# Optimization experiments

Hardware: AMD Instinct MI355X
Metric: run time of the kernel (lower is better)

Reference implementation:

```python
import jax, jax.numpy as jnp
import numpy as np

B = 1024      # batch
DIN = 103     # generator/encoder input dim
L1, L2 = 64, 32   # encoder layer widths (latent = 32)
E = 8         # NUM_EXPERTS
GH = 64       # gating hidden width
H = 256       # generator hidden width
DOUT = 51     # generator output dim
EPS = 1e-5    # BatchNorm eps


def setup_inputs() -> dict:
    key = jax.random.key(0)
    ks = jax.random.split(key, 24)
    s = 0.05
    f32 = jnp.float32
    return {
        "x": jax.random.normal(ks[0], (B, DIN), f32),
        # encoder Linear + BN params
        "w1": jax.random.normal(ks[1], (L1, DIN), f32) * s,
        "b1": jnp.zeros((L1,), f32),
        "gamma1": jnp.ones((L1,), f32),
        "beta1": jnp.zeros((L1,), f32),
        "w2": jax.random.normal(ks[2], (L2, L1), f32) * s,
        "b2": jnp.zeros((L2,), f32),
        "gamma2": jnp.ones((L2,), f32),
        "beta2": jnp.zeros((L2,), f32),
        # gating MLP (latent 32 -> GH -> GH -> E, ELU, softmax)
        "gw1": jax.random.normal(ks[3], (GH, L2), f32) * s,
        "gb1": jnp.zeros((GH,), f32),
        "gw2": jax.random.normal(ks[4], (GH, GH), f32) * s,
        "gb2": jnp.zeros((GH,), f32),
        "gw3": jax.random.normal(ks[5], (E, GH), f32) * s,
        "gb3": jnp.zeros((E,), f32),
        # expert weight banks for 3-layer generator (MANN style)
        "ew1": jax.random.normal(ks[6], (E, DIN, H), f32) * s,
        "eb1": jnp.zeros((E, H), f32),
        "ew2": jax.random.normal(ks[7], (E, H, H), f32) * s,
        "eb2": jnp.zeros((E, H), f32),
        "ew3": jax.random.normal(ks[8], (E, H, DOUT), f32) * s,
        "eb3": jnp.zeros((E, DOUT), f32),
    }


def _batchnorm(h, gamma, beta):
    # training-mode BatchNorm1d: per-batch mean/var (biased var, matching torch)
    m = jnp.mean(h, axis=0)
    v = jnp.mean((h - m) ** 2, axis=0)
    return gamma * (h - m) * jax.lax.rsqrt(v + EPS) + beta


def reference(x, w1, b1, gamma1, beta1, w2, b2, gamma2, beta2,
              gw1, gb1, gw2, gb2, gw3, gb3,
              ew1, eb1, ew2, eb2, ew3, eb3):
    # in-place scale of last 3 features (x[:,100:103] *= 100)
    xs = x.at[:, 100:103].multiply(100.0)
    # encoder: Linear -> BN -> ReLU, twice
    h = jax.nn.relu(_batchnorm(xs @ w1.T + b1, gamma1, beta1))
    latent = jax.nn.relu(_batchnorm(h @ w2.T + b2, gamma2, beta2))
    # gating network -> blending coefficients BC [B, E]
    g = jax.nn.elu(latent @ gw1.T + gb1)
    g = jax.nn.elu(g @ gw2.T + gb2)
    bc = jax.nn.softmax(g @ gw3.T + gb3, axis=-1)
    # MANN-style generator: per-sample expert-blended weights
    wb1 = jnp.einsum('be,eih->bih', bc, ew1)   # [B, DIN, H]
    h1 = jax.nn.elu(jnp.einsum('bi,bih->bh', xs, wb1) + bc @ eb1)
    wb2 = jnp.einsum('be,ehk->bhk', bc, ew2)   # [B, H, H]
    h2 = jax.nn.elu(jnp.einsum('bh,bhk->bk', h1, wb2) + bc @ eb2)
    wb3 = jnp.einsum('be,eho->bho', bc, ew3)   # [B, H, DOUT]
    out = jnp.einsum('bh,bho->bo', h2, wb3) + bc @ eb3
    return out
```

## Files before the change

### kernel.cpp

```cpp
#include <hip/hip_runtime.h>
#include <math.h>


#define DIN 103
#define NE  8
#define HH  256
#define DOUT 51
#define EPSBN 1e-5f

typedef __attribute__((ext_vector_type(8))) short bf16x8;
typedef __attribute__((ext_vector_type(4))) float f32x4;
typedef __attribute__((ext_vector_type(8))) unsigned short us8;
typedef unsigned short ushort_t;

__device__ __forceinline__ float eluf(float v) { return v > 0.f ? v : (expf(v) - 1.f); }
__device__ __forceinline__ unsigned short bf16h(float f) {
  unsigned u = __float_as_uint(f);
  u += 0x7FFFu + ((u >> 16) & 1u);
  return (unsigned short)(u >> 16);
}
__device__ __forceinline__ float bf16f(unsigned short h) { return __uint_as_float(((unsigned)h) << 16); }
__device__ __forceinline__ void split_bf16(float v, unsigned short& h, unsigned short& l) {
  h = bf16h(v);
  l = bf16h(v - bf16f(h));
}
#define MFMA __builtin_amdgcn_mfma_f32_16x16x32_bf16

#define O_SLOTS1 0
#define O_SLOTS2 8192
#define O_H1RAW  20480
#define O_H2RAW  86016
#define O_XSH    118784
#define O_XSL    184320
#define O_E1H    258048
#define O_E1L    389120
#define O_E2H    520192
#define O_E3H    782336

__global__ __launch_bounds__(256) void k_prep_enc1(
    const float* __restrict__ x, const float* __restrict__ w1, const float* __restrict__ b1,
    const float* __restrict__ ew1, const float* __restrict__ ew2, const float* __restrict__ ew3,
    float* __restrict__ ws) {
  __shared__ union {
    float tile[32][65];
    float xt[16][104];
    struct { float w1L[64 * DIN]; float xr[16][104]; float hb[16][64]; } e1;
  } sm;
  int bk = blockIdx.x, t = threadIdx.x;
  int l2 = t & 63, c = l2 & 15, q = l2 >> 4;

  if (bk < 256) {
    int nh = bk & 3, kc = (bk >> 2) & 7, e = bk >> 5;
    int k0 = kc * 32, n0 = nh * 64;
#pragma unroll
    for (int i = 0; i < 8; ++i) {
      int kl = (t >> 6) + i * 4;
      sm.tile[kl][t & 63] = ew2[((size_t)e * HH + k0 + kl) * HH + n0 + (t & 63)];
    }
    __syncthreads();
    int nsl = t >> 6;
    us8 H8;
#pragma unroll
    for (int j = 0; j < 8; ++j) H8[j] = bf16h(sm.tile[q * 8 + j][nsl * 16 + c]);
    size_t dst = (((size_t)(e * 16 + nh * 4 + nsl)) * 8 + kc) * 512 + l2 * 8;
    *(us8*)((ushort_t*)(ws + O_E2H) + dst) = H8;
  } else if (bk < 384) {
    int b2 = bk - 256;
    int nh = b2 & 3, kc = (b2 >> 2) & 3, e = b2 >> 4;
    int k0 = kc * 32, n0 = nh * 64;
#pragma unroll
    for (int i = 0; i < 8; ++i) {
      int kl = (t >> 6) + i * 4;
      int k = k0 + kl;
      sm.tile[kl][t & 63] = (k < DIN) ? ew1[((size_t)e * DIN + k) * HH + n0 + (t & 63)] : 0.f;
    }
    __syncthreads();
    int nsl = t >> 6;
    us8 H8, L8;
#pragma unroll
    for (int j = 0; j < 8; ++j) {
      unsigned short h, lo; split_bf16(sm.tile[q * 8 + j][nsl * 16 + c], h, lo);
      H8[j] = h; L8[j] = lo;
    }
    size_t dst = (((size_t)(e * 16 + nh * 4 + nsl)) * 4 + kc) * 512 + l2 * 8;
    *(us8*)((ushort_t*)(ws + O_E1H) + dst) = H8;
    *(us8*)((ushort_t*)(ws + O_E1L) + dst) = L8;
  } else if (bk < 448) {
    int b2 = bk - 384;
    int kc = b2 & 7, e = b2 >> 3;
    int k0 = kc * 32;
#pragma unroll
    for (int i = 0; i < 8; ++i) {
      int kl = (t >> 6) + i * 4;
      int n = t & 63;
      sm.tile[kl][n] = (n < DOUT) ? ew3[((size_t)e * HH + k0 + kl) * DOUT + n] : 0.f;
    }
    __syncthreads();
    int nsl = t >> 6;
    us8 H8;
#pragma unroll
    for (int j = 0; j < 8; ++j) H8[j] = bf16h(sm.tile[q * 8 + j][nsl * 16 + c]);
    size_t dst = (((size_t)(e * 4 + nsl)) * 8 + kc) * 512 + l2 * 8;
    *(us8*)((ushort_t*)(ws + O_E3H) + dst) = H8;
  } else if (bk < 512) {
    int msub = bk - 448;
    for (int i = t; i < 16 * 104; i += 256) {
      int b = i / 104, k = i - b * 104;
      float v = 0.f;
      if (k < DIN) { v = x[(size_t)(msub * 16 + b) * DIN + k]; if (k >= 100) v *= 100.f; }
      sm.xt[b][k] = v;
    }
    __syncthreads();
    int kc = t >> 6;
    int m = c;
    us8 H8, L8;
#pragma unroll
    for (int j = 0; j < 8; ++j) {
      int k = kc * 32 + q * 8 + j;
      float v = (k < 104) ? sm.xt[m][k] : 0.f;
      unsigned short h, lo; split_bf16(v, h, lo);
      H8[j] = h; L8[j] = lo;
    }
    size_t dst = ((size_t)msub * 4 + kc) * 512 + l2 * 8;
    *(us8*)((ushort_t*)(ws + O_XSH) + dst) = H8;
    *(us8*)((ushort_t*)(ws + O_XSL) + dst) = L8;
  } else {
    float* slots1 = ws + O_SLOTS1;
    float* h1raw  = ws + O_H1RAW;
    int bkl = bk - 512;
    int r0 = bkl * 16;
    for (int i = t; i < 64 * DIN; i += 256) sm.e1.w1L[i] = w1[i];
    for (int i = t; i < 16 * 104; i += 256) {
      int r = i / 104, c2 = i - r * 104;
      float v = 0.f;
      if (c2 < DIN) { v = x[(size_t)(r0 + r) * DIN + c2]; if (c2 >= 100) v *= 100.f; }
      sm.e1.xr[r][c2] = v;
    }
    __syncthreads();
#pragma unroll
    for (int i = 0; i < 4; ++i) {
      int idx = t + i * 256;
      int r = idx >> 6, j = idx & 63;
      float acc = b1[j];
      for (int k = 0; k < DIN; ++k) acc = fmaf(sm.e1.xr[r][k], sm.e1.w1L[j * DIN + k], acc);
      sm.e1.hb[r][j] = acc;
      h1raw[(size_t)(r0 + r) * 64 + j] = acc;
    }
    __syncthreads();
    if (t < 64) {
      float s = 0.f, qq = 0.f;
      for (int r = 0; r < 16; ++r) { float v = sm.e1.hb[r][t]; s += v; qq += v * v; }
      slots1[bkl * 128 + t] = s;
      slots1[bkl * 128 + 64 + t] = qq;
    }
  }
}

__global__ __launch_bounds__(256) void k_enc2(
    const float* __restrict__ gamma1, const float* __restrict__ beta1,
    const float* __restrict__ w2, const float* __restrict__ b2, float* __restrict__ ws) {
  __shared__ float w2T[64 * 33];
  __shared__ float red[128];
  __shared__ float sc1[64], sh1[64];
  __shared__ float h1b[16][64];
  __shared__ float hb2[16][32];
  float* slots1 = ws + O_SLOTS1;
  float* slots2 = ws + O_SLOTS2;
  float* h1raw  = ws + O_H1RAW;
  float* h2raw  = ws + O_H2RAW;
  int bk = blockIdx.x, t = threadIdx.x;
  int R0 = bk * 16;
  for (int i = t; i < 2048; i += 256) { int j = i >> 6, k = i & 63; w2T[k * 33 + j] = w2[i]; }
  if (t < 128) {
    float s = 0.f;
    for (int b = 0; b < 64; ++b) s += slots1[b * 128 + t];
    red[t] = s;
  }
  __syncthreads();
  if (t < 64) {
    float m = red[t] * (1.f / 1024.f);
    float v = red[64 + t] * (1.f / 1024.f) - m * m;
    float sc = gamma1[t] * rsqrtf(v + EPSBN);
    sc1[t] = sc; sh1[t] = beta1[t] - m * sc;
  }
  __syncthreads();
#pragma unroll
  for (int i = 0; i < 4; ++i) {
    int idx = t + i * 256;
    int r = idx >> 6, k = idx & 63;
    h1b[r][k] = fmaxf(fmaf(h1raw[(size_t)(R0 + r) * 64 + k], sc1[k], sh1[k]), 0.f);
  }
  __syncthreads();
#pragma unroll
  for (int i = 0; i < 2; ++i) {
    int o = t + i * 256;
    int r = o >> 5, j = o & 31;
    float acc = b2[j];
    for (int k = 0; k < 64; ++k) acc = fmaf(h1b[r][k], w2T[k * 33 + j], acc);
    hb2[r][j] = acc;
    h2raw[(size_t)(R0 + r) * 32 + j] = acc;
  }
  __syncthreads();
  if (t < 32) {
    float s = 0.f, q = 0.f;
    for (int r = 0; r < 16; ++r) { float v = hb2[r][t]; s += v; q += v * v; }
    slots2[bk * 64 + t] = s;
    slots2[bk * 64 + 32 + t] = q;
  }
}

__global__ __launch_bounds__(512) void k_mega(
    const float* __restrict__ gamma2, const float* __restrict__ beta2,
    const float* __restrict__ gw1, const float* __restrict__ gb1,
    const float* __restrict__ gw2, const float* __restrict__ gb2,
    const float* __restrict__ gw3, const float* __restrict__ gb3,
    const float* __restrict__ eb1, const float* __restrict__ eb2,
    const float* __restrict__ eb3,
    const float* __restrict__ ws, float* __restrict__ out) {
  __shared__ union {
    struct {
      float gw1L[64 * 33];
      float gw2L[64 * 65];
      float gw3L[8 * 65];
      float gb1L[64], gb2L[64], gb3L[8];
      float red2[64], sc2[32], sh2[32];
      float lat[16][32];
      float g1[16][64], g2[16][64];
    } gate;
    struct {
      float hT[256][17];
      float eb[2048];
    } comb;
    struct {
      float p3s[8][16][64];
      float eb3L[8][64];
    } g3;
  } U;
  __shared__ us8 aHv[512], aLv[512];
  __shared__ float bcL[16][8];

  const int bk = blockIdx.x, t = threadIdx.x;
  const int wv = t >> 6, l = t & 63, c = l & 15, quad = l >> 4;
  const int R0 = bk * 16;
  const float* slots2 = ws + O_SLOTS2;
  const float* h2raw  = ws + O_H2RAW;
  const ushort_t* XsH = (const ushort_t*)(ws + O_XSH);
  const ushort_t* XsL = (const ushort_t*)(ws + O_XSL);
  const ushort_t* E1H = (const ushort_t*)(ws + O_E1H);
  const ushort_t* E1L = (const ushort_t*)(ws + O_E1L);
  const ushort_t* E2H = (const ushort_t*)(ws + O_E2H);
  const ushort_t* E3H = (const ushort_t*)(ws + O_E3H);

  for (int i = t; i < 2048; i += 512) { int j = i >> 5, k = i & 31; U.gate.gw1L[j * 33 + k] = gw1[i]; }
  for (int i = t; i < 4096; i += 512) { int j = i >> 6, k = i & 63; U.gate.gw2L[j * 65 + k] = gw2[i]; }
  { int j = t >> 6, k = t & 63; U.gate.gw3L[j * 65 + k] = gw3[t]; }
  if (t < 64) { U.gate.gb1L[t] = gb1[t]; U.gate.gb2L[t] = gb2[t]; }
  if (t < 8) U.gate.gb3L[t] = gb3[t];
  if (t < 64) {
    float s = 0.f;
    for (int b = 0; b < 64; ++b) s += slots2[b * 64 + t];
    U.gate.red2[t] = s;
  }
  __syncthreads();
  if (t < 32) {
    float m = U.gate.red2[t] * (1.f / 1024.f);
    float v = U.gate.red2[32 + t] * (1.f / 1024.f) - m * m;
    float sc = gamma2[t] * rsqrtf(v + EPSBN);
    U.gate.sc2[t] = sc; U.gate.sh2[t] = beta2[t] - m * sc;
  }
  __syncthreads();
  { int r = t >> 5, cc = t & 31;
    U.gate.lat[r][cc] = fmaxf(fmaf(h2raw[(size_t)(R0 + r) * 32 + cc], U.gate.sc2[cc], U.gate.sh2[cc]), 0.f); }
  __syncthreads();
#pragma unroll
  for (int rr = 0; rr < 2; ++rr) {
    int r = wv * 2 + rr;
    float a1 = U.gate.gb1L[l];
    for (int k = 0; k < 32; ++k) a1 = fmaf(U.gate.gw1L[l * 33 + k], U.gate.lat[r][k], a1);
    U.gate.g1[r][l] = eluf(a1);
  }
  __syncthreads();
#pragma unroll
  for (int rr = 0; rr < 2; ++rr) {
    int r = wv * 2 + rr;
    float a2 = U.gate.gb2L[l];
    for (int k = 0; k < 64; ++k) a2 = fmaf(U.gate.gw2L[l * 65 + k], U.gate.g1[r][k], a2);
    U.gate.g2[r][l] = eluf(a2);
  }
  __syncthreads();
#pragma unroll
  for (int rr = 0; rr < 2; ++rr) {
    int r = wv * 2 + rr;
    if (l < 8) {
      float a3 = U.gate.gb3L[l];
      for (int k = 0; k < 64; ++k) a3 = fmaf(U.gate.gw3L[l * 65 + k], U.gate.g2[r][k], a3);
      float mx = a3;
      mx = fmaxf(mx, __shfl_xor(mx, 1));
      mx = fmaxf(mx, __shfl_xor(mx, 2));
      mx = fmaxf(mx, __shfl_xor(mx, 4));
      float p = expf(a3 - mx);
      float sp = p;
      sp += __shfl_xor(sp, 1); sp += __shfl_xor(sp, 2); sp += __shfl_xor(sp, 4);
      bcL[r][l] = p / sp;
    }
  }
  __syncthreads();

  for (int i = t; i < 2048; i += 512) U.comb.eb[i] = eb1[i];
  bf16x8 a1h[4], a1l[4];
#pragma unroll
  for (int kc = 0; kc < 4; ++kc) {
    a1h[kc] = *(const bf16x8*)(XsH + ((size_t)bk * 4 + kc) * 512 + l * 8);
    a1l[kc] = *(const bf16x8*)(XsL + ((size_t)bk * 4 + kc) * 512 + l * 8);
  }
  __syncthreads();
  {
    f32x4 blend[2] = {};
#pragma unroll
    for (int e = 0; e < NE; ++e) {
      float bcv[4];
#pragma unroll
      for (int r = 0; r < 4; ++r) bcv[r] = bcL[quad * 4 + r][e];
#pragma unroll
      for (int nsi = 0; nsi < 2; ++nsi) {
        int ns = wv * 2 + nsi;
        f32x4 acc = {};
#pragma unroll
        for (int kc = 0; kc < 4; ++kc) {
          size_t bo = (((size_t)(e * 16 + ns)) * 4 + kc) * 512 + l * 8;
          bf16x8 bh = *(const bf16x8*)(E1H + bo);
          bf16x8 bl = *(const bf16x8*)(E1L + bo);
          acc = MFMA(a1h[kc], bh, acc, 0, 0, 0);
          acc = MFMA(a1l[kc], bh, acc, 0, 0, 0);
          acc = MFMA(a1h[kc], bl, acc, 0, 0, 0);
        }
        float ebv = U.comb.eb[e * HH + ns * 16 + c];
#pragma unroll
        for (int r = 0; r < 4; ++r) blend[nsi][r] = fmaf(bcv[r], acc[r] + ebv, blend[nsi][r]);
      }
    }
#pragma unroll
    for (int nsi = 0; nsi < 2; ++nsi) {
      int col = (wv * 2 + nsi) * 16 + c;
#pragma unroll
      for (int r = 0; r < 4; ++r) U.comb.hT[col][quad * 4 + r] = eluf(blend[nsi][r]);
    }
  }
  __syncthreads();
  {
    int l2 = t & 63, row = l2 & 15, k0 = (t >> 6) * 32 + (l2 >> 4) * 8;
    us8 H, L;
#pragma unroll
    for (int j = 0; j < 8; ++j) {
      unsigned short h, lo; split_bf16(U.comb.hT[k0 + j][row], h, lo);
      H[j] = h; L[j] = lo;
    }
    aHv[t] = H; aLv[t] = L;
  }
  __syncthreads();

  for (int i = t; i < 2048; i += 512) U.comb.eb[i] = eb2[i];
  bf16x8 a2h[8], a2l[8];
#pragma unroll
  for (int kc = 0; kc < 8; ++kc) {
    a2h[kc] = *(const bf16x8*)&aHv[kc * 64 + l];
    a2l[kc] = *(const bf16x8*)&aLv[kc * 64 + l];
  }
  __syncthreads();
  {
    f32x4 blend[2] = {};
#pragma unroll
    for (int e = 0; e < NE; ++e) {
      float bcv[4];
#pragma unroll
      for (int r = 0; r < 4; ++r) bcv[r] = bcL[quad * 4 + r][e];
#pragma unroll
      for (int nsi = 0; nsi < 2; ++nsi) {
        int ns = wv * 2 + nsi;
        f32x4 acc = {};
#pragma unroll
        for (int kc = 0; kc < 8; ++kc) {
          size_t bo = (((size_t)(e * 16 + ns)) * 8 + kc) * 512 + l * 8;
          bf16x8 bh = *(const bf16x8*)(E2H + bo);
          acc = MFMA(a2h[kc], bh, acc, 0, 0, 0);
          acc = MFMA(a2l[kc], bh, acc, 0, 0, 0);
        }
        float ebv = U.comb.eb[e * HH + ns * 16 + c];
#pragma unroll
        for (int r = 0; r < 4; ++r) blend[nsi][r] = fmaf(bcv[r], acc[r] + ebv, blend[nsi][r]);
      }
    }
#pragma unroll
    for (int nsi = 0; nsi < 2; ++nsi) {
      int col = (wv * 2 + nsi) * 16 + c;
#pragma unroll
      for (int r = 0; r < 4; ++r) U.comb.hT[col][quad * 4 + r] = eluf(blend[nsi][r]);
    }
  }
  __syncthreads();
  {
    int l2 = t & 63, row = l2 & 15, k0 = (t >> 6) * 32 + (l2 >> 4) * 8;
    us8 H, L;
#pragma unroll
    for (int j = 0; j < 8; ++j) {
      unsigned short h, lo; split_bf16(U.comb.hT[k0 + j][row], h, lo);
      H[j] = h; L[j] = lo;
    }
    aHv[t] = H; aLv[t] = L;
  }
  __syncthreads();

  { int e = t >> 6, n = t & 63; U.g3.eb3L[e][n] = (n < DOUT) ? eb3[e * DOUT + n] : 0.f; }
  {
    const int e = wv;
    f32x4 acc[4] = {};
#pragma unroll
    for (int kc = 0; kc < 8; ++kc) {
      bf16x8 ah = *(const bf16x8*)&aHv[kc * 64 + l];
      bf16x8 al = *(const bf16x8*)&aLv[kc * 64 + l];
#pragma unroll
      for (int nsi = 0; nsi < 4; ++nsi) {
        size_t bo = (((size_t)(e * 4 + nsi)) * 8 + kc) * 512 + l * 8;
        bf16x8 bh = *(const bf16x8*)(E3H + bo);
        acc[nsi] = MFMA(ah, bh, acc[nsi], 0, 0, 0);
        acc[nsi] = MFMA(al, bh, acc[nsi], 0, 0, 0);
      }
    }
#pragma unroll
    for (int nsi = 0; nsi < 4; ++nsi)
#pragma unroll
      for (int r = 0; r < 4; ++r)
        U.g3.p3s[e][quad * 4 + r][nsi * 16 + c] = acc[nsi][r];
  }
  __syncthreads();
#pragma unroll
  for (int i = 0; i < 2; ++i) {
    int idx = t + i * 512;
    int row = idx >> 6, col = idx & 63;
    float s = 0.f;
#pragma unroll
    for (int e2 = 0; e2 < 8; ++e2)
      s = fmaf(bcL[row][e2], U.g3.p3s[e2][row][col] + U.g3.eb3L[e2][col], s);
    if (col < DOUT) out[(size_t)(R0 + row) * DOUT + col] = s;
  }
}

extern "C" void kernel_launch(void* const* d_in, const int* in_sizes, int n_in,
                              void* d_out, int out_size, void* d_ws, size_t ws_size,
                              hipStream_t stream) {
  const float* x      = (const float*)d_in[0];
  const float* w1     = (const float*)d_in[1];
  const float* b1     = (const float*)d_in[2];
  const float* gamma1 = (const float*)d_in[3];
  const float* beta1  = (const float*)d_in[4];
  const float* w2     = (const float*)d_in[5];
  const float* b2     = (const float*)d_in[6];
  const float* gamma2 = (const float*)d_in[7];
  const float* beta2  = (const float*)d_in[8];
  const float* gw1    = (const float*)d_in[9];
  const float* gb1    = (const float*)d_in[10];
  const float* gw2    = (const float*)d_in[11];
  const float* gb2    = (const float*)d_in[12];
  const float* gw3    = (const float*)d_in[13];
  const float* gb3    = (const float*)d_in[14];
  const float* ew1    = (const float*)d_in[15];
  const float* eb1    = (const float*)d_in[16];
  const float* ew2    = (const float*)d_in[17];
  const float* eb2    = (const float*)d_in[18];
  const float* ew3    = (const float*)d_in[19];
  const float* eb3    = (const float*)d_in[20];
  float* wsf  = (float*)d_ws;
  float* outp = (float*)d_out;

  k_prep_enc1<<<576, 256, 0, stream>>>(x, w1, b1, ew1, ew2, ew3, wsf);
  k_enc2<<<64, 256, 0, stream>>>(gamma1, beta1, w2, b2, wsf);
  k_mega<<<64, 512, 0, stream>>>(gamma2, beta2, gw1, gb1, gw2, gb2, gw3, gb3,
                                 eb1, eb2, eb3, wsf, outp);
}
```

Before: 156.7 us.

## Fuse enc2 into mega kernel via software grid barrier and L2 prefetch

Removes the separate enc2 kernel launch by computing the second encoder layer inside the mega kernel. A hierarchical atomic grid barrier across the 64 blocks makes the BN2 batch statistics complete before gating starts, and the pre-BN h2 values now stay in shared memory instead of going through global memory. Before the barrier, each block reads a slice of the expert weight workspace into a discarded sum so those weights are warm in cache. The change relies on all 64 blocks being co-resident, which holds at this grid size, and adds barrier spin time plus extra reads for the prefetch.

```diff
diff --git a/kernel.cpp b/kernel.cpp
--- a/kernel.cpp
+++ b/kernel.cpp
@@ -26,16 +26,50 @@
 }
 #define MFMA __builtin_amdgcn_mfma_f32_16x16x32_bf16
 
+__device__ __forceinline__ void stA(float* p, float v) {
+  __hip_atomic_store(p, v, __ATOMIC_RELAXED, __HIP_MEMORY_SCOPE_AGENT);
+}
+__device__ __forceinline__ float ldA(const float* p) {
+  return __hip_atomic_load((float*)p, __ATOMIC_RELAXED, __HIP_MEMORY_SCOPE_AGENT);
+}
+__device__ __forceinline__ void stAu(unsigned* p, unsigned v) {
+  __hip_atomic_store(p, v, __ATOMIC_RELAXED, __HIP_MEMORY_SCOPE_AGENT);
+}
+__device__ __forceinline__ unsigned ldAu(const unsigned* p) {
+  return __hip_atomic_load((unsigned*)p, __ATOMIC_RELAXED, __HIP_MEMORY_SCOPE_AGENT);
+}
+
 #define O_SLOTS1 0
 #define O_SLOTS2 8192
 #define O_H1RAW  20480
-#define O_H2RAW  86016
 #define O_XSH    118784
 #define O_XSL    184320
 #define O_E1H    258048
 #define O_E1L    389120
 #define O_E2H    520192
 #define O_E3H    782336
+#define O_ESPAN  589824
+#define O_BAR    1372160
+
+__device__ __forceinline__ void gbar64(unsigned* base, int blk) {
+  asm volatile("s_waitcnt vmcnt(0)" ::: "memory");
+  __syncthreads();
+  if (threadIdx.x == 0) {
+    unsigned a = __hip_atomic_fetch_add(base + (blk >> 3) * 32, 1u,
+                                        __ATOMIC_RELAXED, __HIP_MEMORY_SCOPE_AGENT);
+    if (a == 7u) {
+      unsigned r = __hip_atomic_fetch_add(base + 256, 1u,
+                                          __ATOMIC_RELAXED, __HIP_MEMORY_SCOPE_AGENT);
+      if (r == 7u) {
+#pragma unroll
+        for (int j = 0; j < 8; ++j) stAu(base + 288 + j * 32, 1u);
+      }
+    }
+    while (ldAu(base + 288 + (blk & 7) * 32) == 0u)
+      __builtin_amdgcn_s_sleep(2);
+  }
+  __syncthreads();
+}
 
 __global__ __launch_bounds__(256) void k_prep_enc1(
     const float* __restrict__ x, const float* __restrict__ w1, const float* __restrict__ b1,
@@ -48,6 +82,11 @@
   } sm;
   int bk = blockIdx.x, t = threadIdx.x;
   int l2 = t & 63, c = l2 & 15, q = l2 >> 4;
+  if (bk == 0) {
+    unsigned* bz = (unsigned*)(ws + O_BAR);
+#pragma unroll
+    for (int i = 0; i < 4; ++i) bz[t + i * 256] = 0u;
+  }
 
   if (bk < 256) {
     int nh = bk & 3, kc = (bk >> 2) & 7, e = bk >> 5;
@@ -156,94 +195,34 @@
   }
 }
 
-__global__ __launch_bounds__(256) void k_enc2(
+__global__ __launch_bounds__(512) void k_mega(
     const float* __restrict__ gamma1, const float* __restrict__ beta1,
-    const float* __restrict__ w2, const float* __restrict__ b2, float* __restrict__ ws) {
-  __shared__ float w2T[64 * 33];
-  __shared__ float red[128];
-  __shared__ float sc1[64], sh1[64];
-  __shared__ float h1b[16][64];
-  __shared__ float hb2[16][32];
-  float* slots1 = ws + O_SLOTS1;
-  float* slots2 = ws + O_SLOTS2;
-  float* h1raw  = ws + O_H1RAW;
-  float* h2raw  = ws + O_H2RAW;
-  int bk = blockIdx.x, t = threadIdx.x;
-  int R0 = bk * 16;
-  for (int i = t; i < 2048; i += 256) { int j = i >> 6, k = i & 63; w2T[k * 33 + j] = w2[i]; }
-  if (t < 128) {
-    float s = 0.f;
-    for (int b = 0; b < 64; ++b) s += slots1[b * 128 + t];
-    red[t] = s;
-  }
-  __syncthreads();
-  if (t < 64) {
-    float m = red[t] * (1.f / 1024.f);
-    float v = red[64 + t] * (1.f / 1024.f) - m * m;
-    float sc = gamma1[t] * rsqrtf(v + EPSBN);
-    sc1[t] = sc; sh1[t] = beta1[t] - m * sc;
-  }
-  __syncthreads();
-#pragma unroll
-  for (int i = 0; i < 4; ++i) {
-    int idx = t + i * 256;
-    int r = idx >> 6, k = idx & 63;
-    h1b[r][k] = fmaxf(fmaf(h1raw[(size_t)(R0 + r) * 64 + k], sc1[k], sh1[k]), 0.f);
-  }
-  __syncthreads();
-#pragma unroll
-  for (int i = 0; i < 2; ++i) {
-    int o = t + i * 256;
-    int r = o >> 5, j = o & 31;
-    float acc = b2[j];
-    for (int k = 0; k < 64; ++k) acc = fmaf(h1b[r][k], w2T[k * 33 + j], acc);
-    hb2[r][j] = acc;
-    h2raw[(size_t)(R0 + r) * 32 + j] = acc;
-  }
-  __syncthreads();
-  if (t < 32) {
-    float s = 0.f, q = 0.f;
-    for (int r = 0; r < 16; ++r) { float v = hb2[r][t]; s += v; q += v * v; }
-    slots2[bk * 64 + t] = s;
-    slots2[bk * 64 + 32 + t] = q;
-  }
-}
-
-__global__ __launch_bounds__(512) void k_mega(
+    const float* __restrict__ w2, const float* __restrict__ b2,
     const float* __restrict__ gamma2, const float* __restrict__ beta2,
     const float* __restrict__ gw1, const float* __restrict__ gb1,
     const float* __restrict__ gw2, const float* __restrict__ gb2,
     const float* __restrict__ gw3, const float* __restrict__ gb3,
     const float* __restrict__ eb1, const float* __restrict__ eb2,
     const float* __restrict__ eb3,
-    const float* __restrict__ ws, float* __restrict__ out) {
+    float* __restrict__ ws, float* __restrict__ out) {
   __shared__ union {
-    struct {
-      float gw1L[64 * 33];
-      float gw2L[64 * 65];
-      float gw3L[8 * 65];
-      float gb1L[64], gb2L[64], gb3L[8];
-      float red2[64], sc2[32], sh2[32];
-      float lat[16][32];
-      float g1[16][64], g2[16][64];
-    } gate;
-    struct {
-      float hT[256][17];
-      float eb[2048];
-    } comb;
-    struct {
-      float p3s[8][16][64];
-      float eb3L[8][64];
-    } g3;
+    struct { float w2T[64 * 33]; float red[128]; float sc1[64], sh1[64];
+             float h1b[16][64]; } enc2;
+    struct { float gw1L[64 * 33]; float gw2L[64 * 65]; float gw3L[8 * 65];
+             float gb1L[64], gb2L[64], gb3L[8];
+             float red2[64], sc2[32], sh2[32];
+             float lat[16][32]; float g1[16][64], g2[16][64]; } gate;
+    struct { float hT[256][17]; float eb[2048]; } comb;
+    struct { float p3s[8][16][64]; float eb3L[8][64]; } g3;
   } U;
+  __shared__ float hb2s[16][32];
   __shared__ us8 aHv[512], aLv[512];
   __shared__ float bcL[16][8];
 
-  const int bk = blockIdx.x, t = threadIdx.x;
+  const int blk = blockIdx.x, t = threadIdx.x;
   const int wv = t >> 6, l = t & 63, c = l & 15, quad = l >> 4;
-  const int R0 = bk * 16;
-  const float* slots2 = ws + O_SLOTS2;
-  const float* h2raw  = ws + O_H2RAW;
+  const int R0 = blk * 16;
+  unsigned* bar = (unsigned*)(ws + O_BAR);
   const ushort_t* XsH = (const ushort_t*)(ws + O_XSH);
   const ushort_t* XsL = (const ushort_t*)(ws + O_XSL);
   const ushort_t* E1H = (const ushort_t*)(ws + O_E1H);
@@ -251,167 +230,230 @@
   const ushort_t* E2H = (const ushort_t*)(ws + O_E2H);
   const ushort_t* E3H = (const ushort_t*)(ws + O_E3H);
 
-  for (int i = t; i < 2048; i += 512) { int j = i >> 5, k = i & 31; U.gate.gw1L[j * 33 + k] = gw1[i]; }
-  for (int i = t; i < 4096; i += 512) { int j = i >> 6, k = i & 63; U.gate.gw2L[j * 65 + k] = gw2[i]; }
-  { int j = t >> 6, k = t & 63; U.gate.gw3L[j * 65 + k] = gw3[t]; }
-  if (t < 64) { U.gate.gb1L[t] = gb1[t]; U.gate.gb2L[t] = gb2[t]; }
-  if (t < 8) U.gate.gb3L[t] = gb3[t];
-  if (t < 64) {
-    float s = 0.f;
-    for (int b = 0; b < 64; ++b) s += slots2[b * 64 + t];
-    U.gate.red2[t] = s;
-  }
-  __syncthreads();
-  if (t < 32) {
-    float m = U.gate.red2[t] * (1.f / 1024.f);
-    float v = U.gate.red2[32 + t] * (1.f / 1024.f) - m * m;
-    float sc = gamma2[t] * rsqrtf(v + EPSBN);
-    U.gate.sc2[t] = sc; U.gate.sh2[t] = beta2[t] - m * sc;
-  }
-  __syncthreads();
-  { int r = t >> 5, cc = t & 31;
-    U.gate.lat[r][cc] = fmaxf(fmaf(h2raw[(size_t)(R0 + r) * 32 + cc], U.gate.sc2[cc], U.gate.sh2[cc]), 0.f); }
-  __syncthreads();
-#pragma unroll
-  for (int rr = 0; rr < 2; ++rr) {
-    int r = wv * 2 + rr;
-    float a1 = U.gate.gb1L[l];
-    for (int k = 0; k < 32; ++k) a1 = fmaf(U.gate.gw1L[l * 33 + k], U.gate.lat[r][k], a1);
-    U.gate.g1[r][l] = eluf(a1);
-  }
-  __syncthreads();
-#pragma unroll
-  for (int rr = 0; rr < 2; ++rr) {
-    int r = wv * 2 + rr;
-    float a2 = U.gate.gb2L[l];
-    for (int k = 0; k < 64; ++k) a2 = fmaf(U.gate.gw2L[l * 65 + k], U.gate.g1[r][k], a2);
-    U.gate.g2[r][l] = eluf(a2);
-  }
-  __syncthreads();
-#pragma unroll
-  for (int rr = 0; rr < 2; ++rr) {
-    int r = wv * 2 + rr;
-    if (l < 8) {
-      float a3 = U.gate.gb3L[l];
-      for (int k = 0; k < 64; ++k) a3 = fmaf(U.gate.gw3L[l * 65 + k], U.gate.g2[r][k], a3);
-      float mx = a3;
-      mx = fmaxf(mx, __shfl_xor(mx, 1));
-      mx = fmaxf(mx, __shfl_xor(mx, 2));
-      mx = fmaxf(mx, __shfl_xor(mx, 4));
-      float p = expf(a3 - mx);
-      float sp = p;
-      sp += __shfl_xor(sp, 1); sp += __shfl_xor(sp, 2); sp += __shfl_xor(sp, 4);
-      bcL[r][l] = p / sp;
-    }
-  }
-  __syncthreads();
-
-  for (int i = t; i < 2048; i += 512) U.comb.eb[i] = eb1[i];
   bf16x8 a1h[4], a1l[4];
 #pragma unroll
   for (int kc = 0; kc < 4; ++kc) {
-    a1h[kc] = *(const bf16x8*)(XsH + ((size_t)bk * 4 + kc) * 512 + l * 8);
-    a1l[kc] = *(const bf16x8*)(XsL + ((size_t)bk * 4 + kc) * 512 + l * 8);
-  }
-  __syncthreads();
+    a1h[kc] = *(const bf16x8*)(XsH + ((size_t)blk * 4 + kc) * 512 + l * 8);
+    a1l[kc] = *(const bf16x8*)(XsL + ((size_t)blk * 4 + kc) * 512 + l * 8);
+  }
+
   {
-    f32x4 blend[2] = {};
-#pragma unroll
-    for (int e = 0; e < NE; ++e) {
-      float bcv[4];
-#pragma unroll
-      for (int r = 0; r < 4; ++r) bcv[r] = bcL[quad * 4 + r][e];
+    const int slice = blk >> 3;
+    const float4* src = (const float4*)(ws + O_E1H);
+    float ka = 0.f;
+#pragma unroll
+    for (int i = 0; i < 36; ++i) {
+      float4 v = src[(size_t)slice * 18432 + (size_t)i * 512 + t];
+      ka += v.x + v.y + v.z + v.w;
+    }
+    asm volatile("" :: "v"(ka));
+  }
+
+  {
+    const float* slots1 = ws + O_SLOTS1;
+    float* slots2 = ws + O_SLOTS2;
+    const float* h1raw = ws + O_H1RAW;
+    for (int i = t; i < 2048; i += 512) { int j = i >> 6, k = i & 63; U.enc2.w2T[k * 33 + j] = w2[i]; }
+    if (t < 128) {
+      float s = 0.f;
+      for (int b = 0; b < 64; ++b) s += slots1[b * 128 + t];
+      U.enc2.red[t] = s;
+    }
+    __syncthreads();
+    if (t < 64) {
+      float mm = U.enc2.red[t] * (1.f / 1024.f);
+      float v = U.enc2.red[64 + t] * (1.f / 1024.f) - mm * mm;
+      float sc = gamma1[t] * rsqrtf(v + EPSBN);
+      U.enc2.sc1[t] = sc; U.enc2.sh1[t] = beta1[t] - mm * sc;
+    }
+    __syncthreads();
+#pragma unroll
+    for (int i = 0; i < 2; ++i) {
+      int idx = t + i * 512;
+      int r = idx >> 6, k = idx & 63;
+      U.enc2.h1b[r][k] = fmaxf(fmaf(h1raw[(size_t)(R0 + r) * 64 + k], U.enc2.sc1[k], U.enc2.sh1[k]), 0.f);
+    }
+    __syncthreads();
+    {
+      int r = t >> 5, j = t & 31;
+      float acc = b2[j];
+      for (int k = 0; k < 64; ++k) acc = fmaf(U.enc2.h1b[r][k], U.enc2.w2T[k * 33 + j], acc);
+      hb2s[r][j] = acc;
+    }
+    __syncthreads();
+    if (t < 32) {
+      float s = 0.f, q = 0.f;
+      for (int r = 0; r < 16; ++r) { float v = hb2s[r][t]; s += v; q += v * v; }
+      stA(slots2 + blk * 64 + t, s);
+      stA(slots2 + blk * 64 + 32 + t, q);
+    }
+  }
+  gbar64(bar, blk);
+
+  {
+    const float* slots2 = ws + O_SLOTS2;
+    for (int i = t; i < 2048; i += 512) { int j = i >> 5, k = i & 31; U.gate.gw1L[j * 33 + k] = gw1[i]; }
+    for (int i = t; i < 4096; i += 512) { int j = i >> 6, k = i & 63; U.gate.gw2L[j * 65 + k] = gw2[i]; }
+    { int j = t >> 6, k = t & 63; U.gate.gw3L[j * 65 + k] = gw3[t]; }
+    if (t < 64) { U.gate.gb1L[t] = gb1[t]; U.gate.gb2L[t] = gb2[t]; }
+    if (t < 8) U.gate.gb3L[t] = gb3[t];
+    if (t < 64) {
+      float vvv[64];
+#pragma unroll
+      for (int b = 0; b < 64; ++b) vvv[b] = ldA(slots2 + b * 64 + t);
+      float s = 0.f;
+#pragma unroll
+      for (int b = 0; b < 64; ++b) s += vvv[b];
+      U.gate.red2[t] = s;
+    }
+    __syncthreads();
+    if (t < 32) {
+      float mm = U.gate.red2[t] * (1.f / 1024.f);
+      float v = U.gate.red2[32 + t] * (1.f / 1024.f) - mm * mm;
+      float sc = gamma2[t] * rsqrtf(v + EPSBN);
+      U.gate.sc2[t] = sc; U.gate.sh2[t] = beta2[t] - mm * sc;
+    }
+    __syncthreads();
+    { int r = t >> 5, cc = t & 31;
+      U.gate.lat[r][cc] = fmaxf(fmaf(hb2s[r][cc], U.gate.sc2[cc], U.gate.sh2[cc]), 0.f); }
+    __syncthreads();
+#pragma unroll
+    for (int rr = 0; rr < 2; ++rr) {
+      int r = wv * 2 + rr;
+      float a1 = U.gate.gb1L[l];
+      for (int k = 0; k < 32; ++k) a1 = fmaf(U.gate.gw1L[l * 33 + k], U.gate.lat[r][k], a1);
+      U.gate.g1[r][l] = eluf(a1);
+    }
+    __syncthreads();
+#pragma unroll
+    for (int rr = 0; rr < 2; ++rr) {
+      int r = wv * 2 + rr;
+      float a2 = U.gate.gb2L[l];
+      for (int k = 0; k < 64; ++k) a2 = fmaf(U.gate.gw2L[l * 65 + k], U.gate.g1[r][k], a2);
+      U.gate.g2[r][l] = eluf(a2);
+    }
+    __syncthreads();
+#pragma unroll
+    for (int rr = 0; rr < 2; ++rr) {
+      int r = wv * 2 + rr;
+      if (l < 8) {
+        float a3 = U.gate.gb3L[l];
+        for (int k = 0; k < 64; ++k) a3 = fmaf(U.gate.gw3L[l * 65 + k], U.gate.g2[r][k], a3);
+        float mx = a3;
+        mx = fmaxf(mx, __shfl_xor(mx, 1));
+        mx = fmaxf(mx, __shfl_xor(mx, 2));
+        mx = fmaxf(mx, __shfl_xor(mx, 4));
+        float p = expf(a3 - mx);
+        float sp = p;
+        sp += __shfl_xor(sp, 1); sp += __shfl_xor(sp, 2); sp += __shfl_xor(sp, 4);
+        bcL[r][l] = p / sp;
+      }
+    }
+    __syncthreads();
+
+    for (int i = t; i < 2048; i += 512) U.comb.eb[i] = eb1[i];
+    __syncthreads();
+    {
+      f32x4 blend[2] = {};
+#pragma unroll
+      for (int e = 0; e < NE; ++e) {
+        float bcv[4];
+#pragma unroll
+        for (int r = 0; r < 4; ++r) bcv[r] = bcL[quad * 4 + r][e];
+#pragma unroll
+        for (int nsi = 0; nsi < 2; ++nsi) {
+          int ns = wv * 2 + nsi;
+          f32x4 acc = {};
+#pragma unroll
+          for (int kc = 0; kc < 4; ++kc) {
+            size_t bo = (((size_t)(e * 16 + ns)) * 4 + kc) * 512 + l * 8;
+            bf16x8 bh = *(const bf16x8*)(E1H + bo);
+            bf16x8 bl = *(const bf16x8*)(E1L + bo);
+            acc = MFMA(a1h[kc], bh, acc, 0, 0, 0);
+            acc = MFMA(a1l[kc], bh, acc, 0, 0, 0);
+            acc = MFMA(a1h[kc], bl, acc, 0, 0, 0);
+          }
+          float ebv = U.comb.eb[e * HH + ns * 16 + c];
+#pragma unroll
+          for (int r = 0; r < 4; ++r) blend[nsi][r] = fmaf(bcv[r], acc[r] + ebv, blend[nsi][r]);
+        }
+      }
 #pragma unroll
       for (int nsi = 0; nsi < 2; ++nsi) {
-        int ns = wv * 2 + nsi;
-        f32x4 acc = {};
-#pragma unroll
-        for (int kc = 0; kc < 4; ++kc) {
-          size_t bo = (((size_t)(e * 16 + ns)) * 4 + kc) * 512 + l * 8;
-          bf16x8 bh = *(const bf16x8*)(E1H + bo);
-          bf16x8 bl = *(const bf16x8*)(E1L + bo);
-          acc = MFMA(a1h[kc], bh, acc, 0, 0, 0);
-          acc = MFMA(a1l[kc], bh, acc, 0, 0, 0);
-          acc = MFMA(a1h[kc], bl, acc, 0, 0, 0);
+        int col = (wv * 2 + nsi) * 16 + c;
+#pragma unroll
+        for (int r = 0; r < 4; ++r) U.comb.hT[col][quad * 4 + r] = eluf(blend[nsi][r]);
+      }
+    }
+    __syncthreads();
+    {
+      int l2 = t & 63, row = l2 & 15, k0 = (t >> 6) * 32 + (l2 >> 4) * 8;
+      us8 H, L;
+#pragma unroll
+      for (int j = 0; j < 8; ++j) {
+        unsigned short h, lo; split_bf16(U.comb.hT[k0 + j][row], h, lo);
+        H[j] = h; L[j] = lo;
+      }
+      aHv[t] = H; aLv[t] = L;
+    }
+    __syncthreads();
+  }
+
+  {
+    for (int i = t; i < 2048; i += 512) U.comb.eb[i] = eb2[i];
+    bf16x8 a2h[8], a2l[8];
+#pragma unroll
+    for (int kc = 0; kc < 8; ++kc) {
+      a2h[kc] = *(const bf16x8*)&aHv[kc * 64 + l];
+      a2l[kc] = *(const bf16x8*)&aLv[kc * 64 + l];
+    }
+    __syncthreads();
+    {
+      f32x4 blend[2] = {};
+#pragma unroll
+      for (int e = 0; e < NE; ++e) {
+        float bcv[4];
+#pragma unroll
+        for (int r = 0; r < 4; ++r) bcv[r] = bcL[quad * 4 + r][e];
+#pragma unroll
+        for (int nsi = 0; nsi < 2; ++nsi) {
+          int ns = wv * 2 + nsi;
+          f32x4 acc = {};
+#pragma unroll
+          for (int kc = 0; kc < 8; ++kc) {
+            size_t bo = (((size_t)(e * 16 + ns)) * 8 + kc) * 512 + l * 8;
+            bf16x8 bh = *(const bf16x8*)(E2H + bo);
+            acc = MFMA(a2h[kc], bh, acc, 0, 0, 0);
+            acc = MFMA(a2l[kc], bh, acc, 0, 0, 0);
+          }
+          float ebv = U.comb.eb[e * HH + ns * 16 + c];
+#pragma unroll
+          for (int r = 0; r < 4; ++r) blend[nsi][r] = fmaf(bcv[r], acc[r] + ebv, blend[nsi][r]);
         }
-        float ebv = U.comb.eb[e * HH + ns * 16 + c];
-#pragma unroll
-        for (int r = 0; r < 4; ++r) blend[nsi][r] = fmaf(bcv[r], acc[r] + ebv, blend[nsi][r]);
-      }
-    }
-#pragma unroll
-    for (int nsi = 0; nsi < 2; ++nsi) {
-      int col = (wv * 2 + nsi) * 16 + c;
-#pragma unroll
-      for (int r = 0; r < 4; ++r) U.comb.hT[col][quad * 4 + r] = eluf(blend[nsi][r]);
-    }
-  }
-  __syncthreads();
+      }
+#pragma unroll
+      for (int nsi = 0; nsi < 2; ++nsi) {
+        int col = (wv * 2 + nsi) * 16 + c;
+#pragma unroll
+        for (int r = 0; r < 4; ++r) U.comb.hT[col][quad * 4 + r] = eluf(blend[nsi][r]);
+      }
+    }
+    __syncthreads();
+    {
+      int l2 = t & 63, row = l2 & 15, k0 = (t >> 6) * 32 + (l2 >> 4) * 8;
+      us8 H, L;
+#pragma unroll
+      for (int j = 0; j < 8; ++j) {
+        unsigned short h, lo; split_bf16(U.comb.hT[k0 + j][row], h, lo);
+        H[j] = h; L[j] = lo;
+      }
+      aHv[t] = H; aLv[t] = L;
+    }
+    __syncthreads();
+  }
+
   {
-    int l2 = t & 63, row = l2 & 15, k0 = (t >> 6) * 32 + (l2 >> 4) * 8;
-    us8 H, L;
-#pragma unroll
-    for (int j = 0; j < 8; ++j) {
-      unsigned short h, lo; split_bf16(U.comb.hT[k0 + j][row], h, lo);
-      H[j] = h; L[j] = lo;
-    }
-    aHv[t] = H; aLv[t] = L;
-  }
-  __syncthreads();
-
-  for (int i = t; i < 2048; i += 512) U.comb.eb[i] = eb2[i];
-  bf16x8 a2h[8], a2l[8];
-#pragma unroll
-  for (int kc = 0; kc < 8; ++kc) {
-    a2h[kc] = *(const bf16x8*)&aHv[kc * 64 + l];
-    a2l[kc] = *(const bf16x8*)&aLv[kc * 64 + l];
-  }
-  __syncthreads();
-  {
-    f32x4 blend[2] = {};
-#pragma unroll
-    for (int e = 0; e < NE; ++e) {
-      float bcv[4];
-#pragma unroll
-      for (int r = 0; r < 4; ++r) bcv[r] = bcL[quad * 4 + r][e];
-#pragma unroll
-      for (int nsi = 0; nsi < 2; ++nsi) {
-        int ns = wv * 2 + nsi;
-        f32x4 acc = {};
-#pragma unroll
-        for (int kc = 0; kc < 8; ++kc) {
-          size_t bo = (((size_t)(e * 16 + ns)) * 8 + kc) * 512 + l * 8;
-          bf16x8 bh = *(const bf16x8*)(E2H + bo);
-          acc = MFMA(a2h[kc], bh, acc, 0, 0, 0);
-          acc = MFMA(a2l[kc], bh, acc, 0, 0, 0);
-        }
-        float ebv = U.comb.eb[e * HH + ns * 16 + c];
-#pragma unroll
-        for (int r = 0; r < 4; ++r) blend[nsi][r] = fmaf(bcv[r], acc[r] + ebv, blend[nsi][r]);
-      }
-    }
-#pragma unroll
-    for (int nsi = 0; nsi < 2; ++nsi) {
-      int col = (wv * 2 + nsi) * 16 + c;
-#pragma unroll
-      for (int r = 0; r < 4; ++r) U.comb.hT[col][quad * 4 + r] = eluf(blend[nsi][r]);
-    }
-  }
-  __syncthreads();
-  {
-    int l2 = t & 63, row = l2 & 15, k0 = (t >> 6) * 32 + (l2 >> 4) * 8;
-    us8 H, L;
-#pragma unroll
-    for (int j = 0; j < 8; ++j) {
-      unsigned short h, lo; split_bf16(U.comb.hT[k0 + j][row], h, lo);
-      H[j] = h; L[j] = lo;
-    }
-    aHv[t] = H; aLv[t] = L;
-  }
-  __syncthreads();
-
-  { int e = t >> 6, n = t & 63; U.g3.eb3L[e][n] = (n < DOUT) ? eb3[e * DOUT + n] : 0.f; }
-  {
+    { int e = t >> 6, n = t & 63; U.g3.eb3L[e][n] = (n < DOUT) ? eb3[e * DOUT + n] : 0.f; }
     const int e = wv;
     f32x4 acc[4] = {};
 #pragma unroll
@@ -431,17 +473,17 @@
 #pragma unroll
       for (int r = 0; r < 4; ++r)
         U.g3.p3s[e][quad * 4 + r][nsi * 16 + c] = acc[nsi][r];
-  }
-  __syncthreads();
-#pragma unroll
-  for (int i = 0; i < 2; ++i) {
-    int idx = t + i * 512;
-    int row = idx >> 6, col = idx & 63;
-    float s = 0.f;
-#pragma unroll
-    for (int e2 = 0; e2 < 8; ++e2)
-      s = fmaf(bcL[row][e2], U.g3.p3s[e2][row][col] + U.g3.eb3L[e2][col], s);
-    if (col < DOUT) out[(size_t)(R0 + row) * DOUT + col] = s;
+    __syncthreads();
+#pragma unroll
+    for (int i = 0; i < 2; ++i) {
+      int idx = t + i * 512;
+      int row = idx >> 6, col = idx & 63;
+      float s = 0.f;
+#pragma unroll
+      for (int e2 = 0; e2 < 8; ++e2)
+        s = fmaf(bcL[row][e2], U.g3.p3s[e2][row][col] + U.g3.eb3L[e2][col], s);
+      if (col < DOUT) out[(size_t)(R0 + row) * DOUT + col] = s;
+    }
   }
 }
 
@@ -473,7 +515,7 @@
   float* outp = (float*)d_out;
 
   k_prep_enc1<<<576, 256, 0, stream>>>(x, w1, b1, ew1, ew2, ew3, wsf);
-  k_enc2<<<64, 256, 0, stream>>>(gamma1, beta1, w2, b2, wsf);
-  k_mega<<<64, 512, 0, stream>>>(gamma2, beta2, gw1, gb1, gw2, gb2, gw3, gb3,
+  k_mega<<<64, 512, 0, stream>>>(gamma1, beta1, w2, b2, gamma2, beta2,
+                                 gw1, gb1, gw2, gb2, gw3, gb3,
                                  eb1, eb2, eb3, wsf, outp);
 }
```

New measurement: 151.2 us. -3.5%, faster.
